# Kernel optimization log

Hardware: AMD Instinct MI355X
Metric: run time of the kernel (lower is better)

The kernel has to match this reference:

```python
import jax, jax.numpy as jnp
import numpy as np

N_NODES = 50000
N_EDGES = 1250000
VOCAB = 50000
EMBED = 64
HIDDEN = 64
NUM_REL = 3
N_CLASSES = 2
N_GRAPHS = 512


def setup_inputs() -> dict:
    key = jax.random.key(0)
    ks = jax.random.split(key, 12)
    x = jax.random.randint(ks[0], (N_NODES,), 0, VOCAB, dtype=jnp.int32)
    edge_index = jax.random.randint(ks[1], (2, N_EDGES), 0, N_NODES, dtype=jnp.int32)
    edge_type = jax.random.randint(ks[2], (N_EDGES,), 0, NUM_REL, dtype=jnp.int32)
    batch = jnp.sort(jax.random.randint(ks[3], (N_NODES,), 0, N_GRAPHS, dtype=jnp.int32))
    s = 0.05
    emb = jax.random.normal(ks[4], (VOCAB, EMBED), jnp.float32) * s
    w1_rel = jax.random.normal(ks[5], (NUM_REL, EMBED, HIDDEN), jnp.float32) * s
    w1_root = jax.random.normal(ks[6], (EMBED, HIDDEN), jnp.float32) * s
    b1 = jnp.zeros((HIDDEN,), jnp.float32)
    w2_rel = jax.random.normal(ks[7], (NUM_REL, HIDDEN, HIDDEN), jnp.float32) * s
    w2_root = jax.random.normal(ks[8], (HIDDEN, HIDDEN), jnp.float32) * s
    b2 = jnp.zeros((HIDDEN,), jnp.float32)
    lin_w = jax.random.normal(ks[9], (HIDDEN, N_CLASSES), jnp.float32) * s
    lin_b = jnp.zeros((N_CLASSES,), jnp.float32)
    return {"x": x, "edge_index": edge_index, "edge_type": edge_type, "batch": batch,
            "emb": emb, "w1_rel": w1_rel, "w1_root": w1_root, "b1": b1,
            "w2_rel": w2_rel, "w2_root": w2_root, "b2": b2,
            "lin_w": lin_w, "lin_b": lin_b}


def rgcn_conv(h, src, dst, edge_type, w_rel, w_root, bias):
    # PyG RGCNConv: out = h @ W_root + bias + sum_r mean-aggregated (h_src @ W_r)
    out = h @ w_root + bias
    h_src = h[src]  # [E, F] gather
    for r in range(NUM_REL):
        mask = (edge_type == r).astype(h.dtype)  # [E]
        m = (h_src @ w_rel[r]) * mask[:, None]   # [E, H]
        s = jax.ops.segment_sum(m, dst, num_segments=N_NODES)
        cnt = jax.ops.segment_sum(mask, dst, num_segments=N_NODES)
        out = out + s / jnp.maximum(cnt, 1.0)[:, None]
    return out


def reference(x, edge_index, edge_type, batch, emb, w1_rel, w1_root, b1,
              w2_rel, w2_root, b2, lin_w, lin_b):
    src, dst = edge_index[0], edge_index[1]
    emb_eff = emb.at[0].set(0.0)  # padding_idx=0
    h = emb_eff[x]  # [N, EMBED]
    h = jax.nn.relu(rgcn_conv(h, src, dst, edge_type, w1_rel, w1_root, b1))
    h = jax.nn.relu(rgcn_conv(h, src, dst, edge_type, w2_rel, w2_root, b2))
    # global mean pool over graphs
    sums = jax.ops.segment_sum(h, batch, num_segments=N_GRAPHS)
    cnt = jax.ops.segment_sum(jnp.ones((h.shape[0],), h.dtype), batch, num_segments=N_GRAPHS)
    pooled = sums / jnp.maximum(cnt, 1.0)[:, None]  # [G, HIDDEN]
    return pooled @ lin_w + lin_b  # [G, N_CLASSES]
```

## Files before the change

kernel.cpp:

```cpp
#include <hip/hip_runtime.h>

#define CHUNK 2048

__global__ __launch_bounds__(256) void embed_count_kernel(
    const int* __restrict__ x, const float* __restrict__ emb, float* __restrict__ h0,
    const int* __restrict__ ei, int* __restrict__ pcount,
    int n_nodes, int n_edges, int n_bkt, int embed_blocks)
{
    __shared__ int cnt[512];
    int t = threadIdx.x;
    if ((int)blockIdx.x < embed_blocks) {
        int tt = blockIdx.x * 256 + t;
        if (tt < n_nodes * 16) {
            int n = tt >> 4, q = tt & 15;
            int xv = x[n];
            float4 v = {0.f, 0.f, 0.f, 0.f};
            if (xv != 0) v = *(const float4*)(emb + (size_t)xv * 64 + q * 4);
            *(float4*)(h0 + (size_t)n * 64 + q * 4) = v;
        }
        return;
    }
    int jb = blockIdx.x - embed_blocks;
    for (int b = t; b < 512; b += 256) cnt[b] = 0;
    __syncthreads();
    int base = jb * CHUNK;
#pragma unroll
    for (int i = 0; i < CHUNK / 256; ++i) {
        int e = base + i * 256 + t;
        if (e < n_edges) atomicAdd(&cnt[ei[n_edges + e] >> 7], 1);
    }
    __syncthreads();
    for (int b = t; b < n_bkt; b += 256) pcount[jb * n_bkt + b] = cnt[b];
}

__global__ __launch_bounds__(256) void colscan_kernel(
    const int* __restrict__ pcount, int* __restrict__ pre,
    int* __restrict__ totals, int* __restrict__ rowstartR,
    const int* __restrict__ batch, const float* __restrict__ linb,
    float* __restrict__ inv_cnt, float* __restrict__ outg,
    int n_chk, int n_bkt, int n_edges, int n_nodes, int n_graphs)
{
    __shared__ int ps[256];
    int b = blockIdx.x, t = threadIdx.x;
    if (b >= n_bkt) {
        int g = (b - n_bkt) * 256 + t;
        if (g < n_graphs) {
            int lo = 0, hi = n_nodes;
            while (lo < hi) { int mid = (lo + hi) >> 1; if (batch[mid] < g) lo = mid + 1; else hi = mid; }
            int s = lo;
            lo = 0; hi = n_nodes;
            while (lo < hi) { int mid = (lo + hi) >> 1; if (batch[mid] < g + 1) lo = mid + 1; else hi = mid; }
            inv_cnt[g] = 1.f / (float)max(lo - s, 1);
            outg[2 * g + 0] = linb[0];
            outg[2 * g + 1] = linb[1];
        }
        return;
    }
    if (b == 0 && t == 0) rowstartR[4 * n_nodes] = n_edges;
    int v[4], s = 0;
#pragma unroll
    for (int i = 0; i < 4; ++i) {
        int jj = t * 4 + i;
        v[i] = (jj < n_chk) ? pcount[jj * n_bkt + b] : 0;
        s += v[i];
    }
    ps[t] = s;
    __syncthreads();
    for (int o = 1; o < 256; o <<= 1) {
        int u = (t >= o) ? ps[t - o] : 0;
        __syncthreads();
        ps[t] += u;
        __syncthreads();
    }
    int run = (t > 0) ? ps[t - 1] : 0;
#pragma unroll
    for (int i = 0; i < 4; ++i) {
        int jj = t * 4 + i;
        if (jj < n_chk) pre[jj * n_bkt + b] = run;
        run += v[i];
    }
    if (t == 255) totals[b] = run;
}

__global__ __launch_bounds__(256) void scatter_kernel(
    const int* __restrict__ ei, const int* __restrict__ et,
    const int* __restrict__ pre, const int* __restrict__ totals,
    int* __restrict__ esort, int* __restrict__ bucket_start,
    int n_edges, int n_bkt)
{
    __shared__ int bs[512], fill2[512], ps[256];
    int t = threadIdx.x, j = blockIdx.x;
    int a0 = (2 * t < n_bkt) ? totals[2 * t] : 0;
    int a1 = (2 * t + 1 < n_bkt) ? totals[2 * t + 1] : 0;
    ps[t] = a0 + a1;
    __syncthreads();
    for (int o = 1; o < 256; o <<= 1) {
        int u = (t >= o) ? ps[t - o] : 0;
        __syncthreads();
        ps[t] += u;
        __syncthreads();
    }
    int basex = (t > 0) ? ps[t - 1] : 0;
    bs[2 * t] = basex;
    bs[2 * t + 1] = basex + a0;
    fill2[t] = 0; fill2[t + 256] = 0;
    __syncthreads();
    if (j == 0) {
        for (int b = t; b < n_bkt; b += 256) bucket_start[b] = bs[b];
        if (t == 0) bucket_start[n_bkt] = n_edges;
    }
    for (int b = t; b < n_bkt; b += 256) bs[b] += pre[j * n_bkt + b];
    __syncthreads();
    int base = j * CHUNK;
#pragma unroll
    for (int i = 0; i < CHUNK / 256; ++i) {
        int e = base + i * 256 + t;
        if (e < n_edges) {
            int s = ei[e], d = ei[n_edges + e], r = et[e];
            int b = d >> 7;
            int pos = bs[b] + atomicAdd(&fill2[b], 1);
            esort[pos] = s | (r << 16) | ((d & 127) << 18);
        }
    }
}

__global__ __launch_bounds__(256) void bucket_sort_kernel(
    const int* __restrict__ bucket_start, int* __restrict__ esort,
    int* __restrict__ scratch, int* __restrict__ rowstartR, int n_nodes)
{
    __shared__ int cnt[512], off[512], fill[512], ps[256];
    int t = threadIdx.x, b = blockIdx.x;
    int s = bucket_start[b], e = bucket_start[b + 1];
    cnt[t] = 0; cnt[t + 256] = 0; fill[t] = 0; fill[t + 256] = 0;
    __syncthreads();
    int* scr = scratch + (size_t)b * 8192;
    for (int i = s + t; i < e; i += 256) {
        int p = esort[i];
        scr[i - s] = p;
        atomicAdd(&cnt[(p >> 16) & 0x1FF], 1);
    }
    __syncthreads();
    int a0 = cnt[2 * t], a1 = cnt[2 * t + 1];
    ps[t] = a0 + a1;
    __syncthreads();
    for (int o = 1; o < 256; o <<= 1) {
        int v = (t >= o) ? ps[t - o] : 0;
        __syncthreads();
        ps[t] += v;
        __syncthreads();
    }
    int basex = (t > 0) ? ps[t - 1] : 0;
    off[2 * t] = basex;
    off[2 * t + 1] = basex + a0;
    __syncthreads();
    int d0 = b * 128 + (2 * t >> 2);
    if (d0 < n_nodes) rowstartR[b * 512 + 2 * t] = s + off[2 * t];
    int d1 = b * 128 + ((2 * t + 1) >> 2);
    if (d1 < n_nodes) rowstartR[b * 512 + 2 * t + 1] = s + off[2 * t + 1];
    __syncthreads();
    for (int i = s + t; i < e; i += 256) {
        int p = scr[i - s];
        int bin = (p >> 16) & 0x1FF;
        int pos = s + off[bin] + atomicAdd(&fill[bin], 1);
        esort[pos] = p;
    }
}

__global__ __launch_bounds__(256) void agg_kernel(
    const float* __restrict__ hin, const int* __restrict__ rowstartR,
    const int* __restrict__ esort, float* __restrict__ means, int n_nodes)
{
    int wid = (blockIdx.x * 256 + threadIdx.x) >> 6;
    int lane = threadIdx.x & 63;
    if (wid >= n_nodes) return;
    int q = lane >> 4;
    int c = lane & 15;
    int4 rs = *(const int4*)(rowstartR + wid * 4);
    int s = rs.x, e = rs.w;

    float4 a0 = {0.f,0.f,0.f,0.f}, a1 = {0.f,0.f,0.f,0.f}, a2 = {0.f,0.f,0.f,0.f};

    int i = s + 4 * q;
    for (; i + 4 <= e; i += 16) {
        int p0 = esort[i], p1 = esort[i + 1], p2 = esort[i + 2], p3 = esort[i + 3];
        float4 v0 = *(const float4*)(hin + (size_t)(p0 & 0xFFFF) * 64 + c * 4);
        float4 v1 = *(const float4*)(hin + (size_t)(p1 & 0xFFFF) * 64 + c * 4);
        float4 v2 = *(const float4*)(hin + (size_t)(p2 & 0xFFFF) * 64 + c * 4);
        float4 v3 = *(const float4*)(hin + (size_t)(p3 & 0xFFFF) * 64 + c * 4);
#pragma unroll
        for (int m = 0; m < 4; ++m) {
            int p = m == 0 ? p0 : m == 1 ? p1 : m == 2 ? p2 : p3;
            float4 v = m == 0 ? v0 : m == 1 ? v1 : m == 2 ? v2 : v3;
            int r = (p >> 16) & 3;
            float m0 = (r == 0) ? 1.f : 0.f;
            float m1 = (r == 1) ? 1.f : 0.f;
            float m2 = (r == 2) ? 1.f : 0.f;
            a0.x = fmaf(m0, v.x, a0.x); a0.y = fmaf(m0, v.y, a0.y);
            a0.z = fmaf(m0, v.z, a0.z); a0.w = fmaf(m0, v.w, a0.w);
            a1.x = fmaf(m1, v.x, a1.x); a1.y = fmaf(m1, v.y, a1.y);
            a1.z = fmaf(m1, v.z, a1.z); a1.w = fmaf(m1, v.w, a1.w);
            a2.x = fmaf(m2, v.x, a2.x); a2.y = fmaf(m2, v.y, a2.y);
            a2.z = fmaf(m2, v.z, a2.z); a2.w = fmaf(m2, v.w, a2.w);
        }
    }
#pragma unroll
    for (int m = 0; m < 3; ++m) {
        int ii = i + m;
        if (ii < e) {
            int p = esort[ii];
            float4 v = *(const float4*)(hin + (size_t)(p & 0xFFFF) * 64 + c * 4);
            int r = (p >> 16) & 3;
            float m0 = (r == 0) ? 1.f : 0.f;
            float m1 = (r == 1) ? 1.f : 0.f;
            float m2 = (r == 2) ? 1.f : 0.f;
            a0.x = fmaf(m0, v.x, a0.x); a0.y = fmaf(m0, v.y, a0.y);
            a0.z = fmaf(m0, v.z, a0.z); a0.w = fmaf(m0, v.w, a0.w);
            a1.x = fmaf(m1, v.x, a1.x); a1.y = fmaf(m1, v.y, a1.y);
            a1.z = fmaf(m1, v.z, a1.z); a1.w = fmaf(m1, v.w, a1.w);
            a2.x = fmaf(m2, v.x, a2.x); a2.y = fmaf(m2, v.y, a2.y);
            a2.z = fmaf(m2, v.z, a2.z); a2.w = fmaf(m2, v.w, a2.w);
        }
    }
#pragma unroll
    for (int off = 16; off < 64; off <<= 1) {
        a0.x += __shfl_xor(a0.x, off); a0.y += __shfl_xor(a0.y, off);
        a0.z += __shfl_xor(a0.z, off); a0.w += __shfl_xor(a0.w, off);
        a1.x += __shfl_xor(a1.x, off); a1.y += __shfl_xor(a1.y, off);
        a1.z += __shfl_xor(a1.z, off); a1.w += __shfl_xor(a1.w, off);
        a2.x += __shfl_xor(a2.x, off); a2.y += __shfl_xor(a2.y, off);
        a2.z += __shfl_xor(a2.z, off); a2.w += __shfl_xor(a2.w, off);
    }
    if (q < 3) {
        int cnt = (q == 0) ? (rs.y - rs.x) : (q == 1) ? (rs.z - rs.y) : (rs.w - rs.z);
        float4 a = (q == 0) ? a0 : (q == 1) ? a1 : a2;
        float inv = 1.f / (float)max(cnt, 1);
        float4 m = {a.x * inv, a.y * inv, a.z * inv, a.w * inv};
        *(float4*)(means + (size_t)wid * 192 + q * 64 + c * 4) = m;
    }
}

__device__ __forceinline__ void stage16(const float* gsrc, float* ldst)
{
    __builtin_amdgcn_global_load_lds(
        (const __attribute__((address_space(1))) unsigned int*)gsrc,
        (__attribute__((address_space(3))) unsigned int*)ldst,
        16, 0, 0);
}

__global__ __launch_bounds__(256, 6) void transform_kernel(
    const float* __restrict__ hin, const float* __restrict__ means,
    const float* __restrict__ wroot, const float* __restrict__ wrel,
    const float* __restrict__ bias, float* __restrict__ hout,
    const int* __restrict__ batch, const float* __restrict__ linw,
    const float* __restrict__ inv_cnt, float* __restrict__ outg,
    int n_nodes, int do_pool)
{
    __shared__ float wsh[2][2048];
    __shared__ float gacc[64][2];
    int t = threadIdx.x;
    int gt = blockIdx.x * 256 + t;
    int g = gt >> 4, q = gt & 15;
    int n0 = g * 2;
    bool active = (n0 < n_nodes);

    stage16(wroot + t * 4,        wsh[0] + t * 4);
    stage16(wroot + 1024 + t * 4, wsh[0] + 1024 + t * 4);

    float4 acc0, acc1;
    {
        float4 b = {0.f, 0.f, 0.f, 0.f};
        if (active) b = *(const float4*)(bias + q * 4);
        acc0 = b; acc1 = b;
    }

    const float* hv = hin + (size_t)n0 * 64;
    const float* mv = means + (size_t)n0 * 192;

    for (int ss = 0; ss < 8; ++ss) {
        __syncthreads();
        if (ss < 7) {
            const float* wsrc = (ss + 1 < 2) ? (wroot + (size_t)(ss + 1) * 2048)
                                             : (wrel + (size_t)(ss - 1) * 2048);
            float* d = wsh[(ss + 1) & 1];
            stage16(wsrc + t * 4,        d + t * 4);
            stage16(wsrc + 1024 + t * 4, d + 1024 + t * 4);
        }
        int p = ss >> 1;
        const float* vbase = ((p == 0) ? hv : (mv + (p - 1) * 64)) + (ss & 1) * 32;
        int vstride = (p == 0) ? 64 : 192;
        const float* wbuf = wsh[ss & 1];
        if (active) {
#pragma unroll 2
            for (int k4 = 0; k4 < 8; ++k4) {
                float4 v0 = *(const float4*)(vbase + k4 * 4);
                float4 v1 = *(const float4*)(vbase + vstride + k4 * 4);
#pragma unroll
                for (int kk = 0; kk < 4; ++kk) {
                    float4 w = *(const float4*)(wbuf + (k4 * 4 + kk) * 64 + q * 4);
                    float s0 = kk == 0 ? v0.x : kk == 1 ? v0.y : kk == 2 ? v0.z : v0.w;
                    float s1 = kk == 0 ? v1.x : kk == 1 ? v1.y : kk == 2 ? v1.z : v1.w;
                    acc0.x = fmaf(s0, w.x, acc0.x);
                    acc0.y = fmaf(s0, w.y, acc0.y);
                    acc0.z = fmaf(s0, w.z, acc0.z);
                    acc0.w = fmaf(s0, w.w, acc0.w);
                    acc1.x = fmaf(s1, w.x, acc1.x);
                    acc1.y = fmaf(s1, w.y, acc1.y);
                    acc1.z = fmaf(s1, w.z, acc1.z);
                    acc1.w = fmaf(s1, w.w, acc1.w);
                }
            }
        }
    }
    if (!do_pool) {
        if (active) {
            float* o = hout + (size_t)n0 * 64 + q * 4;
            float4 r0 = {fmaxf(acc0.x, 0.f), fmaxf(acc0.y, 0.f),
                         fmaxf(acc0.z, 0.f), fmaxf(acc0.w, 0.f)};
            float4 r1 = {fmaxf(acc1.x, 0.f), fmaxf(acc1.y, 0.f),
                         fmaxf(acc1.z, 0.f), fmaxf(acc1.w, 0.f)};
            *(float4*)(o) = r0;
            *(float4*)(o + 64) = r1;
        }
    } else {
        if (t < 64) { gacc[t][0] = 0.f; gacc[t][1] = 0.f; }
        __syncthreads();
        int nbase = blockIdx.x * 32;
        int gmin = batch[min(nbase, n_nodes - 1)];
        if (active) {
            float4 lwA = *(const float4*)(linw + q * 8);
            float4 lwB = *(const float4*)(linw + q * 8 + 4);
            float d0[2], d1[2];
            {
                float4 r = {fmaxf(acc0.x, 0.f), fmaxf(acc0.y, 0.f),
                            fmaxf(acc0.z, 0.f), fmaxf(acc0.w, 0.f)};
                d0[0] = r.x * lwA.x + r.y * lwA.z + r.z * lwB.x + r.w * lwB.z;
                d1[0] = r.x * lwA.y + r.y * lwA.w + r.z * lwB.y + r.w * lwB.w;
            }
            {
                float4 r = {fmaxf(acc1.x, 0.f), fmaxf(acc1.y, 0.f),
                            fmaxf(acc1.z, 0.f), fmaxf(acc1.w, 0.f)};
                d0[1] = r.x * lwA.x + r.y * lwA.z + r.z * lwB.x + r.w * lwB.z;
                d1[1] = r.x * lwA.y + r.y * lwA.w + r.z * lwB.y + r.w * lwB.w;
            }
#pragma unroll
            for (int off = 1; off < 16; off <<= 1) {
#pragma unroll
                for (int i = 0; i < 2; ++i) {
                    d0[i] += __shfl_xor(d0[i], off);
                    d1[i] += __shfl_xor(d1[i], off);
                }
            }
            if (q == 0) {
#pragma unroll
                for (int i = 0; i < 2; ++i) {
                    int n = n0 + i;
                    if (n < n_nodes) {
                        int gg = batch[n];
                        float ic = inv_cnt[gg];
                        int idx = gg - gmin;
                        if (idx < 64) {
                            atomicAdd(&gacc[idx][0], d0[i] * ic);
                            atomicAdd(&gacc[idx][1], d1[i] * ic);
                        } else {
                            atomicAdd(&outg[2 * gg + 0], d0[i] * ic);
                            atomicAdd(&outg[2 * gg + 1], d1[i] * ic);
                        }
                    }
                }
            }
        }
        __syncthreads();
        if (t < 64) {
            float v0 = gacc[t][0], v1 = gacc[t][1];
            if (v0 != 0.f || v1 != 0.f) {
                atomicAdd(&outg[2 * (gmin + t) + 0], v0);
                atomicAdd(&outg[2 * (gmin + t) + 1], v1);
            }
        }
    }
}

extern "C" void kernel_launch(void* const* d_in, const int* in_sizes, int n_in,
                              void* d_out, int out_size, void* d_ws, size_t ws_size,
                              hipStream_t stream)
{
    const int*   x      = (const int*)d_in[0];
    const int*   ei     = (const int*)d_in[1];
    const int*   et     = (const int*)d_in[2];
    const int*   batch  = (const int*)d_in[3];
    const float* emb    = (const float*)d_in[4];
    const float* w1rel  = (const float*)d_in[5];
    const float* w1root = (const float*)d_in[6];
    const float* b1     = (const float*)d_in[7];
    const float* w2rel  = (const float*)d_in[8];
    const float* w2root = (const float*)d_in[9];
    const float* b2     = (const float*)d_in[10];
    const float* linw   = (const float*)d_in[11];
    const float* linb   = (const float*)d_in[12];
    float* out = (float*)d_out;

    const int N = in_sizes[0];
    const int E = in_sizes[2];
    const int G = out_size / 2;
    const int NBKT = (N + 127) >> 7;
    const int NCHK = (E + CHUNK - 1) / CHUNK;

    float* hA        = (float*)d_ws;
    float* hB        = hA + (size_t)N * 64;
    float* means     = hB + (size_t)N * 64;
    int*   esort     = (int*)(means + (size_t)N * 192);
    int*   rowstartR = esort + E;
    int*   bucket_start = rowstartR + 4 * N + 4;
    int*   totals    = bucket_start + NBKT + 1;
    float* inv_cnt   = (float*)(totals + NBKT);
    int*   scratch   = (int*)means;
    int*   pcount    = (int*)means + 4 * 1024 * 1024;
    int*   pre       = (int*)means + 5 * 1024 * 1024;

    int embedBlocks = (N * 16 + 255) / 256;
    embed_count_kernel<<<embedBlocks + NCHK, 256, 0, stream>>>(
        x, emb, hA, ei, pcount, N, E, NBKT, embedBlocks);
    int gBlocks = (G + 255) / 256;
    colscan_kernel<<<NBKT + gBlocks, 256, 0, stream>>>(
        pcount, pre, totals, rowstartR, batch, linb, inv_cnt, out,
        NCHK, NBKT, E, N, G);
    scatter_kernel<<<NCHK, 256, 0, stream>>>(ei, et, pre, totals, esort, bucket_start, E, NBKT);
    bucket_sort_kernel<<<NBKT, 256, 0, stream>>>(bucket_start, esort, scratch, rowstartR, N);

    int aggBlocks = (N * 64 + 255) / 256;
    int tfBlocks  = ((N + 1) / 2 * 16 + 255) / 256;
    agg_kernel<<<aggBlocks, 256, 0, stream>>>(hA, rowstartR, esort, means, N);
    transform_kernel<<<tfBlocks, 256, 0, stream>>>(
        hA, means, w1root, w1rel, b1, hB, batch, linw, inv_cnt, out, N, 0);
    agg_kernel<<<aggBlocks, 256, 0, stream>>>(hB, rowstartR, esort, means, N);
    transform_kernel<<<tfBlocks, 256, 0, stream>>>(
        hB, means, w2root, w2rel, b2, hA, batch, linw, inv_cnt, out, N, 1);
}
```

Measured before the change: 299.4 us.

## Widen aggregation unroll, derive relation-0 sum algebraically, read weights directly from global

The aggregation kernel now handles 8 edges per lane group per iteration instead of 4, which puts more gathers in flight. It accumulates the total sum and recovers the relation-0 sum by subtracting the relation-1 and relation-2 sums, cutting the per-edge FMAs. The transform kernel drops the double-buffered LDS weight staging and its per-stage barriers, loading the weights straight from global memory through the cache. Risks include slight floating-point differences from the subtraction and more register pressure from the wider unroll. The weight reads now depend on cache hits rather than shared memory.

```diff
diff --git a/kernel.cpp b/kernel.cpp
--- a/kernel.cpp
+++ b/kernel.cpp
@@ -180,47 +180,45 @@
 
     float4 a0 = {0.f,0.f,0.f,0.f}, a1 = {0.f,0.f,0.f,0.f}, a2 = {0.f,0.f,0.f,0.f};
 
-    int i = s + 4 * q;
-    for (; i + 4 <= e; i += 16) {
-        int p0 = esort[i], p1 = esort[i + 1], p2 = esort[i + 2], p3 = esort[i + 3];
-        float4 v0 = *(const float4*)(hin + (size_t)(p0 & 0xFFFF) * 64 + c * 4);
-        float4 v1 = *(const float4*)(hin + (size_t)(p1 & 0xFFFF) * 64 + c * 4);
-        float4 v2 = *(const float4*)(hin + (size_t)(p2 & 0xFFFF) * 64 + c * 4);
-        float4 v3 = *(const float4*)(hin + (size_t)(p3 & 0xFFFF) * 64 + c * 4);
-#pragma unroll
-        for (int m = 0; m < 4; ++m) {
-            int p = m == 0 ? p0 : m == 1 ? p1 : m == 2 ? p2 : p3;
-            float4 v = m == 0 ? v0 : m == 1 ? v1 : m == 2 ? v2 : v3;
-            int r = (p >> 16) & 3;
-            float m0 = (r == 0) ? 1.f : 0.f;
-            float m1 = (r == 1) ? 1.f : 0.f;
-            float m2 = (r == 2) ? 1.f : 0.f;
-            a0.x = fmaf(m0, v.x, a0.x); a0.y = fmaf(m0, v.y, a0.y);
-            a0.z = fmaf(m0, v.z, a0.z); a0.w = fmaf(m0, v.w, a0.w);
-            a1.x = fmaf(m1, v.x, a1.x); a1.y = fmaf(m1, v.y, a1.y);
-            a1.z = fmaf(m1, v.z, a1.z); a1.w = fmaf(m1, v.w, a1.w);
-            a2.x = fmaf(m2, v.x, a2.x); a2.y = fmaf(m2, v.y, a2.y);
-            a2.z = fmaf(m2, v.z, a2.z); a2.w = fmaf(m2, v.w, a2.w);
-        }
-    }
-#pragma unroll
-    for (int m = 0; m < 3; ++m) {
+    int i = s + 8 * q;
+    for (; i + 8 <= e; i += 32) {
+        int p[8];
+        float4 v[8];
+#pragma unroll
+        for (int m = 0; m < 8; ++m) p[m] = esort[i + m];
+#pragma unroll
+        for (int m = 0; m < 8; ++m)
+            v[m] = *(const float4*)(hin + (size_t)(p[m] & 0xFFFF) * 64 + c * 4);
+#pragma unroll
+        for (int m = 0; m < 8; ++m) {
+            int r = (p[m] >> 16) & 3;
+            float m1 = (float)(r & 1);
+            float m2 = (float)(r >> 1);
+            a0.x += v[m].x; a0.y += v[m].y; a0.z += v[m].z; a0.w += v[m].w;
+            a1.x = fmaf(m1, v[m].x, a1.x); a1.y = fmaf(m1, v[m].y, a1.y);
+            a1.z = fmaf(m1, v[m].z, a1.z); a1.w = fmaf(m1, v[m].w, a1.w);
+            a2.x = fmaf(m2, v[m].x, a2.x); a2.y = fmaf(m2, v[m].y, a2.y);
+            a2.z = fmaf(m2, v[m].z, a2.z); a2.w = fmaf(m2, v[m].w, a2.w);
+        }
+    }
+#pragma unroll
+    for (int m = 0; m < 7; ++m) {
         int ii = i + m;
         if (ii < e) {
             int p = esort[ii];
             float4 v = *(const float4*)(hin + (size_t)(p & 0xFFFF) * 64 + c * 4);
             int r = (p >> 16) & 3;
-            float m0 = (r == 0) ? 1.f : 0.f;
-            float m1 = (r == 1) ? 1.f : 0.f;
-            float m2 = (r == 2) ? 1.f : 0.f;
-            a0.x = fmaf(m0, v.x, a0.x); a0.y = fmaf(m0, v.y, a0.y);
-            a0.z = fmaf(m0, v.z, a0.z); a0.w = fmaf(m0, v.w, a0.w);
+            float m1 = (float)(r & 1);
+            float m2 = (float)(r >> 1);
+            a0.x += v.x; a0.y += v.y; a0.z += v.z; a0.w += v.w;
             a1.x = fmaf(m1, v.x, a1.x); a1.y = fmaf(m1, v.y, a1.y);
             a1.z = fmaf(m1, v.z, a1.z); a1.w = fmaf(m1, v.w, a1.w);
             a2.x = fmaf(m2, v.x, a2.x); a2.y = fmaf(m2, v.y, a2.y);
             a2.z = fmaf(m2, v.z, a2.z); a2.w = fmaf(m2, v.w, a2.w);
         }
     }
+    a0.x -= a1.x + a2.x; a0.y -= a1.y + a2.y;
+    a0.z -= a1.z + a2.z; a0.w -= a1.w + a2.w;
 #pragma unroll
     for (int off = 16; off < 64; off <<= 1) {
         a0.x += __shfl_xor(a0.x, off); a0.y += __shfl_xor(a0.y, off);
@@ -239,14 +237,6 @@
     }
 }
 
-__device__ __forceinline__ void stage16(const float* gsrc, float* ldst)
-{
-    __builtin_amdgcn_global_load_lds(
-        (const __attribute__((address_space(1))) unsigned int*)gsrc,
-        (__attribute__((address_space(3))) unsigned int*)ldst,
-        16, 0, 0);
-}
-
 __global__ __launch_bounds__(256, 6) void transform_kernel(
     const float* __restrict__ hin, const float* __restrict__ means,
     const float* __restrict__ wroot, const float* __restrict__ wrel,
@@ -255,7 +245,6 @@
     const float* __restrict__ inv_cnt, float* __restrict__ outg,
     int n_nodes, int do_pool)
 {
-    __shared__ float wsh[2][2048];
     __shared__ float gacc[64][2];
     int t = threadIdx.x;
     int gt = blockIdx.x * 256 + t;
@@ -263,9 +252,6 @@
     int n0 = g * 2;
     bool active = (n0 < n_nodes);
 
-    stage16(wroot + t * 4,        wsh[0] + t * 4);
-    stage16(wroot + 1024 + t * 4, wsh[0] + 1024 + t * 4);
-
     float4 acc0, acc1;
     {
         float4 b = {0.f, 0.f, 0.f, 0.f};
@@ -276,27 +262,19 @@
     const float* hv = hin + (size_t)n0 * 64;
     const float* mv = means + (size_t)n0 * 192;
 
-    for (int ss = 0; ss < 8; ++ss) {
-        __syncthreads();
-        if (ss < 7) {
-            const float* wsrc = (ss + 1 < 2) ? (wroot + (size_t)(ss + 1) * 2048)
-                                             : (wrel + (size_t)(ss - 1) * 2048);
-            float* d = wsh[(ss + 1) & 1];
-            stage16(wsrc + t * 4,        d + t * 4);
-            stage16(wsrc + 1024 + t * 4, d + 1024 + t * 4);
-        }
-        int p = ss >> 1;
-        const float* vbase = ((p == 0) ? hv : (mv + (p - 1) * 64)) + (ss & 1) * 32;
-        int vstride = (p == 0) ? 64 : 192;
-        const float* wbuf = wsh[ss & 1];
-        if (active) {
-#pragma unroll 2
-            for (int k4 = 0; k4 < 8; ++k4) {
-                float4 v0 = *(const float4*)(vbase + k4 * 4);
-                float4 v1 = *(const float4*)(vbase + vstride + k4 * 4);
+    if (active) {
+#pragma unroll
+        for (int p = 0; p < 4; ++p) {
+            const float* vb = (p == 0) ? hv : (mv + (p - 1) * 64);
+            int vst = (p == 0) ? 64 : 192;
+            const float* wb = ((p == 0) ? wroot : (wrel + (size_t)(p - 1) * 4096)) + q * 4;
+#pragma unroll 4
+            for (int k4 = 0; k4 < 16; ++k4) {
+                float4 v0 = *(const float4*)(vb + k4 * 4);
+                float4 v1 = *(const float4*)(vb + vst + k4 * 4);
 #pragma unroll
                 for (int kk = 0; kk < 4; ++kk) {
-                    float4 w = *(const float4*)(wbuf + (k4 * 4 + kk) * 64 + q * 4);
+                    float4 w = *(const float4*)(wb + (size_t)(k4 * 4 + kk) * 64);
                     float s0 = kk == 0 ? v0.x : kk == 1 ? v0.y : kk == 2 ? v0.z : v0.w;
                     float s1 = kk == 0 ? v1.x : kk == 1 ? v1.y : kk == 2 ? v1.z : v1.w;
                     acc0.x = fmaf(s0, w.x, acc0.x);
```

New measurement: 404.2 us. 1.35x slower.
